# Optimization experiments

Measured on AMD Instinct MI355X. Metric: run time of the kernel, lower is better.

## Reference

```python
import jax, jax.numpy as jnp
import numpy as np

N_SIN = 3  # fcn_n_sin

def _feats(x):
    # x: [B, Din] -> features [B, Din, 1 + 2*N_SIN]
    omega = (2.0 ** jnp.arange(N_SIN, dtype=x.dtype))  # [n_sin]
    ox = x[..., None] * omega  # [B, Din, n_sin]
    return jnp.concatenate([x[..., None], jnp.sin(ox), jnp.cos(ox)], axis=-1)

def setup_inputs() -> dict:
    key = jax.random.key(0)
    k1, k2, k3 = jax.random.split(key, 3)
    B, Din, Dout, H, F = 2048, 64, 64, 32, 1 + 2 * N_SIN
    x = jax.random.normal(k1, (B, Din), dtype=jnp.float32)
    # xavier-normal-ish init for W1/W2, zeros for biases (matches init_parameters)
    W1 = jax.random.normal(k2, (Din, Dout, H, F), dtype=jnp.float32) * np.sqrt(2.0 / (H + F))
    W2 = jax.random.normal(k3, (Din, Dout, 1, H), dtype=jnp.float32) * np.sqrt(2.0 / (1 + H))
    B1 = jnp.zeros((Din, Dout, H), dtype=jnp.float32)
    B2 = jnp.zeros((Din, Dout, 1), dtype=jnp.float32)
    return {"x": x, "W1": W1, "W2": W2, "B1": B1, "B2": B2}

def reference(x, W1, W2, B1, B2):
    f = _feats(x)  # [B, Din, F]
    # per-edge first layer: [B, Din, Dout, H]
    h = jnp.einsum('bif,iohf->bioh', f, W1) + B1[None]
    h = jax.nn.silu(h)
    # per-edge second layer -> scalar: [B, Din, Dout]
    phis = jnp.einsum('bioh,ioh->bio', h, W2[:, :, 0, :]) + B2[:, :, 0][None]
    return phis.sum(axis=1)  # [B, Dout]
```

## Files before the change

### kernel.cpp

```cpp
#include <hip/hip_runtime.h>
#include <math.h>

typedef _Float16 f16;
typedef f16   f16x4    __attribute__((ext_vector_type(4)));
typedef f16   f16x8    __attribute__((ext_vector_type(8)));
typedef float floatx2  __attribute__((ext_vector_type(2)));
typedef float floatx4  __attribute__((ext_vector_type(4)));
typedef float floatx16 __attribute__((ext_vector_type(16)));

#define LOG2E   1.44269504088896340736f
#define INV_2PI 0.15915494309189533577f

#define B_SZ  2048
#define DIN   64
#define DOUT  64
#define NH    32

#define NIG   4
#define IGW   (DIN / NIG)

#define W1IMG_ELEMS ((size_t)DIN * DOUT * 64 * 4)
#define FIMG_ELEMS  ((size_t)DIN * 64 * 64 * 4)

__device__ __forceinline__ floatx2 pk_add(floatx2 a, floatx2 b) {
    floatx2 d; asm("v_pk_add_f32 %0, %1, %2" : "=v"(d) : "v"(a), "v"(b)); return d;
}
__device__ __forceinline__ floatx2 pk_mul(floatx2 a, floatx2 b) {
    floatx2 d; asm("v_pk_mul_f32 %0, %1, %2" : "=v"(d) : "v"(a), "v"(b)); return d;
}
__device__ __forceinline__ floatx2 pk_fma(floatx2 a, floatx2 b, floatx2 c) {
    floatx2 d; asm("v_pk_fma_f32 %0, %1, %2, %3" : "=v"(d) : "v"(a), "v"(b), "v"(c)); return d;
}

__global__ __launch_bounds__(256) void prep_kernel(
        const float* __restrict__ W1, const float* __restrict__ B1,
        const float* __restrict__ B2, const float* __restrict__ x,
        f16* __restrict__ w1img, f16* __restrict__ fimg,
        float* __restrict__ b2sum, float* __restrict__ out) {
    const int bid = blockIdx.x, tid = threadIdx.x;
    if (bid < 512) {
        int u = bid * 256 + tid;
        int lane2 = u & 31, o = (u >> 5) & 63, i = u >> 11;
        int l0 = lane2 * 2;
        f16x8 v;
        if (lane2 < 16) {
#pragma unroll
            for (int t = 0; t < 2; ++t) {
                const float* w = W1 + (size_t)((i * 64 + o) * 32 + l0 + t) * 7;
#pragma unroll
                for (int j = 0; j < 4; ++j) v[t * 4 + j] = (f16)(w[j] * (-LOG2E));
            }
        } else {
#pragma unroll
            for (int t = 0; t < 2; ++t) {
                int m = l0 - 32 + t;
                const float* w = W1 + (size_t)((i * 64 + o) * 32 + m) * 7;
                v[t * 4 + 0] = (f16)(w[4] * (-LOG2E));
                v[t * 4 + 1] = (f16)(w[5] * (-LOG2E));
                v[t * 4 + 2] = (f16)(w[6] * (-LOG2E));
                v[t * 4 + 3] = (f16)(B1[(i * 64 + o) * 32 + m] * (-LOG2E));
            }
        }
        *(f16x8*)(w1img + (size_t)u * 8) = v;
    } else if (bid < 1024) {
        int u = (bid - 512) * 256 + tid;
        int lane2 = u & 31, btp = (u >> 5) & 63, i = u >> 11;
        int l0 = lane2 * 2;
        f16x8 v;
#pragma unroll
        for (int t = 0; t < 2; ++t) {
            int b = btp * 32 + ((l0 + t) & 31);
            float xv = x[b * 64 + i];
            float s1 = __builtin_amdgcn_sinf(xv * INV_2PI);
            float c1 = __builtin_amdgcn_cosf(xv * INV_2PI);
            float s2 = 2.0f * s1 * c1, c2 = 1.0f - 2.0f * s1 * s1;
            float s4 = 2.0f * s2 * c2, c4 = 1.0f - 2.0f * s2 * s2;
            if (lane2 < 16) { v[t*4+0] = (f16)xv; v[t*4+1] = (f16)s1;
                              v[t*4+2] = (f16)s2; v[t*4+3] = (f16)s4; }
            else            { v[t*4+0] = (f16)c1; v[t*4+1] = (f16)c2;
                              v[t*4+2] = (f16)c4; v[t*4+3] = (f16)1.0f; }
        }
        *(f16x8*)(fimg + (size_t)u * 8) = v;
    } else if (bid < 1152) {
        int t = (bid - 1024) * 256 + tid;
        floatx4 z = {};
        *(floatx4*)(out + (size_t)t * 4) = z;
    } else if (tid < 64) {
        float s = 0.0f;
        for (int i = 0; i < 64; ++i) s += B2[i * 64 + tid];
        b2sum[tid] = s;
    }
}

__device__ __forceinline__ void silu8(
        floatx2 A0, floatx2 A1, floatx2 A2, floatx2 A3,
        floatx2 W0, floatx2 W1, floatx2 W2, floatx2 W3,
        floatx2 one2, float& phi) {
    floatx2 E0 = {__builtin_amdgcn_exp2f(A0[0]), __builtin_amdgcn_exp2f(A0[1])};
    floatx2 E1 = {__builtin_amdgcn_exp2f(A1[0]), __builtin_amdgcn_exp2f(A1[1])};
    floatx2 E2 = {__builtin_amdgcn_exp2f(A2[0]), __builtin_amdgcn_exp2f(A2[1])};
    floatx2 E3 = {__builtin_amdgcn_exp2f(A3[0]), __builtin_amdgcn_exp2f(A3[1])};
    floatx2 D0 = pk_add(E0, one2), D1 = pk_add(E1, one2);
    floatx2 D2 = pk_add(E2, one2), D3 = pk_add(E3, one2);
    floatx2 U0 = pk_mul(A0, W0), U1 = pk_mul(A1, W1);
    floatx2 U2 = pk_mul(A2, W2), U3 = pk_mul(A3, W3);
    floatx2 N01 = pk_fma(U0, D1, pk_mul(U1, D0));
    floatx2 N23 = pk_fma(U2, D3, pk_mul(U3, D2));
    floatx2 P01 = pk_mul(D0, D1), P23 = pk_mul(D2, D3);
    floatx2 N   = pk_fma(N01, P23, pk_mul(N23, P01));
    floatx2 DD  = pk_mul(P01, P23);
    float n8 = __builtin_fmaf(N[0], DD[1], N[1] * DD[0]);
    float d8 = DD[0] * DD[1];
    phi = __builtin_fmaf(n8, __builtin_amdgcn_rcpf(d8), phi);
}

__global__ __launch_bounds__(128, 6) void main_kernel(
        const f16* __restrict__ w1img, const f16* __restrict__ fimg,
        const float* __restrict__ W2, const float* __restrict__ b2sum,
        float* __restrict__ out) {
    const int tid  = threadIdx.x;
    const int lane = tid & 63;
    const int wv   = tid >> 6;
    const int btp  = blockIdx.x & 63;
    const int og   = (blockIdx.x >> 6) & 31;
    const int ig   = blockIdx.x >> 11;
    const int o    = __builtin_amdgcn_readfirstlane(og * 2 + wv);
    const int p    = lane >> 5;
    const size_t ibase = (size_t)ig * IGW;

    __shared__ float ws2[2][IGW + 1][32];
    {
        int idx = tid * 8;
        int wv_ = idx >> 9, ii_ = (idx >> 5) & 15, h_ = idx & 31;
        const float* src = W2 + (ibase + ii_) * 2048
                         + (size_t)(og * 2 + wv_) * 32 + h_;
        *(floatx4*)&ws2[wv_][ii_][h_]     = *(const floatx4*)src;
        *(floatx4*)&ws2[wv_][ii_][h_ + 4] = *(const floatx4*)(src + 4);
    }
    __syncthreads();

    const f16* ap = w1img + ibase * 16384 + ((size_t)o   * 64 + lane) * 4;
    const f16* bp = fimg  + ibase * 16384 + ((size_t)btp * 64 + lane) * 4;

    const floatx16 zeroC = {};
    const floatx2  one2  = {1.0f, 1.0f};
    float phiL = 0.0f, phiH = 0.0f;

    f16x4 a0v = *(const f16x4*)ap;
    f16x4 b0v = *(const f16x4*)bp;
    f16x4 a_n = *(const f16x4*)(ap + 16384);
    f16x4 b_n = *(const f16x4*)(bp + 16384);
    floatx16 Ccur = __builtin_amdgcn_mfma_f32_32x32x8f16(a0v, b0v, zeroC, 0, 0, 0);

#pragma unroll 2
    for (int ii = 0; ii < IGW; ++ii) {
        floatx16 Cn = __builtin_amdgcn_mfma_f32_32x32x8f16(a_n, b_n, zeroC, 0, 0, 0);
        const size_t i2 = (size_t)(ii + 2);
        a_n = *(const f16x4*)(ap + i2 * 16384);
        b_n = *(const f16x4*)(bp + i2 * 16384);

        const float* wrow = &ws2[wv][ii][p * 4];
        const floatx4 W0 = *(const floatx4*)(wrow);
        const floatx4 W1v = *(const floatx4*)(wrow + 8);
        const floatx4 W2v = *(const floatx4*)(wrow + 16);
        const floatx4 W3v = *(const floatx4*)(wrow + 24);

        silu8((floatx2){Ccur[0],  Ccur[1]},  (floatx2){Ccur[4],  Ccur[5]},
              (floatx2){Ccur[8],  Ccur[9]},  (floatx2){Ccur[12], Ccur[13]},
              (floatx2){W0[0], W0[1]}, (floatx2){W1v[0], W1v[1]},
              (floatx2){W2v[0], W2v[1]}, (floatx2){W3v[0], W3v[1]},
              one2, phiL);
        silu8((floatx2){Ccur[2],  Ccur[3]},  (floatx2){Ccur[6],  Ccur[7]},
              (floatx2){Ccur[10], Ccur[11]}, (floatx2){Ccur[14], Ccur[15]},
              (floatx2){W0[2], W0[3]}, (floatx2){W1v[2], W1v[3]},
              (floatx2){W2v[2], W2v[3]}, (floatx2){W3v[2], W3v[3]},
              one2, phiH);

        Ccur = Cn;
    }

    float phi = phiL + phiH;
    phi += __shfl_xor(phi, 32, 64);

    if (lane < 32) {
        float v = phi * (-1.0f / LOG2E) + (1.0f / NIG) * b2sum[o];
        unsafeAtomicAdd(out + (size_t)(btp * 32 + lane) * 64 + o, v);
    }
}

extern "C" void kernel_launch(void* const* d_in, const int* in_sizes, int n_in,
                              void* d_out, int out_size, void* d_ws, size_t ws_size,
                              hipStream_t stream) {
    const float* x  = (const float*)d_in[0];
    const float* W1 = (const float*)d_in[1];
    const float* W2 = (const float*)d_in[2];
    const float* B1 = (const float*)d_in[3];
    const float* B2 = (const float*)d_in[4];
    float* out = (float*)d_out;

    f16*   w1img = (f16*)d_ws;
    f16*   fimg  = w1img + W1IMG_ELEMS;
    float* b2sum = (float*)(fimg + FIMG_ELEMS);

    prep_kernel<<<1153, 256, 0, stream>>>(W1, B1, B2, x, w1img, fimg, b2sum, out);
    main_kernel<<<NIG * 32 * 64, 128, 0, stream>>>(w1img, fimg, W2, b2sum, out);
}
```

Measured before the change: 111.8 us.

## Fold W2 into a second W1 image and compute A*W2 via extra MFMA

```diff
diff --git a/kernel.cpp b/kernel.cpp
--- a/kernel.cpp
+++ b/kernel.cpp
@@ -34,36 +34,44 @@
 
 __global__ __launch_bounds__(256) void prep_kernel(
         const float* __restrict__ W1, const float* __restrict__ B1,
-        const float* __restrict__ B2, const float* __restrict__ x,
-        f16* __restrict__ w1img, f16* __restrict__ fimg,
-        float* __restrict__ b2sum, float* __restrict__ out) {
+        const float* __restrict__ W2, const float* __restrict__ B2,
+        const float* __restrict__ x,
+        f16* __restrict__ w1img, f16* __restrict__ w12img,
+        f16* __restrict__ fimg, float* __restrict__ b2sum,
+        float* __restrict__ out) {
     const int bid = blockIdx.x, tid = threadIdx.x;
-    if (bid < 512) {
-        int u = bid * 256 + tid;
+    if (bid < 1024) {
+        const bool second = bid >= 512;
+        int u = (second ? bid - 512 : bid) * 256 + tid;
         int lane2 = u & 31, o = (u >> 5) & 63, i = u >> 11;
         int l0 = lane2 * 2;
         f16x8 v;
         if (lane2 < 16) {
 #pragma unroll
             for (int t = 0; t < 2; ++t) {
-                const float* w = W1 + (size_t)((i * 64 + o) * 32 + l0 + t) * 7;
+                int m = l0 + t;
+                float sc = -LOG2E;
+                if (second) sc *= W2[(size_t)(i * 64 + o) * 32 + m];
+                const float* w = W1 + (size_t)((i * 64 + o) * 32 + m) * 7;
 #pragma unroll
-                for (int j = 0; j < 4; ++j) v[t * 4 + j] = (f16)(w[j] * (-LOG2E));
+                for (int j = 0; j < 4; ++j) v[t * 4 + j] = (f16)(w[j] * sc);
             }
         } else {
 #pragma unroll
             for (int t = 0; t < 2; ++t) {
                 int m = l0 - 32 + t;
+                float sc = -LOG2E;
+                if (second) sc *= W2[(size_t)(i * 64 + o) * 32 + m];
                 const float* w = W1 + (size_t)((i * 64 + o) * 32 + m) * 7;
-                v[t * 4 + 0] = (f16)(w[4] * (-LOG2E));
-                v[t * 4 + 1] = (f16)(w[5] * (-LOG2E));
-                v[t * 4 + 2] = (f16)(w[6] * (-LOG2E));
-                v[t * 4 + 3] = (f16)(B1[(i * 64 + o) * 32 + m] * (-LOG2E));
+                v[t * 4 + 0] = (f16)(w[4] * sc);
+                v[t * 4 + 1] = (f16)(w[5] * sc);
+                v[t * 4 + 2] = (f16)(w[6] * sc);
+                v[t * 4 + 3] = (f16)(B1[(i * 64 + o) * 32 + m] * sc);
             }
         }
-        *(f16x8*)(w1img + (size_t)u * 8) = v;
-    } else if (bid < 1024) {
-        int u = (bid - 512) * 256 + tid;
+        *(f16x8*)((second ? w12img : w1img) + (size_t)u * 8) = v;
+    } else if (bid < 1536) {
+        int u = (bid - 1024) * 256 + tid;
         int lane2 = u & 31, btp = (u >> 5) & 63, i = u >> 11;
         int l0 = lane2 * 2;
         f16x8 v;
@@ -81,8 +89,8 @@
                               v[t*4+2] = (f16)c4; v[t*4+3] = (f16)1.0f; }
         }
         *(f16x8*)(fimg + (size_t)u * 8) = v;
-    } else if (bid < 1152) {
-        int t = (bid - 1024) * 256 + tid;
+    } else if (bid < 1664) {
+        int t = (bid - 1536) * 256 + tid;
         floatx4 z = {};
         *(floatx4*)(out + (size_t)t * 4) = z;
     } else if (tid < 64) {
@@ -94,7 +102,7 @@
 
 __device__ __forceinline__ void silu8(
         floatx2 A0, floatx2 A1, floatx2 A2, floatx2 A3,
-        floatx2 W0, floatx2 W1, floatx2 W2, floatx2 W3,
+        floatx2 U0, floatx2 U1, floatx2 U2, floatx2 U3,
         floatx2 one2, float& phi) {
     floatx2 E0 = {__builtin_amdgcn_exp2f(A0[0]), __builtin_amdgcn_exp2f(A0[1])};
     floatx2 E1 = {__builtin_amdgcn_exp2f(A1[0]), __builtin_amdgcn_exp2f(A1[1])};
@@ -102,8 +110,6 @@
     floatx2 E3 = {__builtin_amdgcn_exp2f(A3[0]), __builtin_amdgcn_exp2f(A3[1])};
     floatx2 D0 = pk_add(E0, one2), D1 = pk_add(E1, one2);
     floatx2 D2 = pk_add(E2, one2), D3 = pk_add(E3, one2);
-    floatx2 U0 = pk_mul(A0, W0), U1 = pk_mul(A1, W1);
-    floatx2 U2 = pk_mul(A2, W2), U3 = pk_mul(A3, W3);
     floatx2 N01 = pk_fma(U0, D1, pk_mul(U1, D0));
     floatx2 N23 = pk_fma(U2, D3, pk_mul(U3, D2));
     floatx2 P01 = pk_mul(D0, D1), P23 = pk_mul(D2, D3);
@@ -115,8 +121,8 @@
 }
 
 __global__ __launch_bounds__(128, 6) void main_kernel(
-        const f16* __restrict__ w1img, const f16* __restrict__ fimg,
-        const float* __restrict__ W2, const float* __restrict__ b2sum,
+        const f16* __restrict__ w1img, const f16* __restrict__ w12img,
+        const f16* __restrict__ fimg, const float* __restrict__ b2sum,
         float* __restrict__ out) {
     const int tid  = threadIdx.x;
     const int lane = tid & 63;
@@ -125,58 +131,40 @@
     const int og   = (blockIdx.x >> 6) & 31;
     const int ig   = blockIdx.x >> 11;
     const int o    = __builtin_amdgcn_readfirstlane(og * 2 + wv);
-    const int p    = lane >> 5;
     const size_t ibase = (size_t)ig * IGW;
 
-    __shared__ float ws2[2][IGW + 1][32];
-    {
-        int idx = tid * 8;
-        int wv_ = idx >> 9, ii_ = (idx >> 5) & 15, h_ = idx & 31;
-        const float* src = W2 + (ibase + ii_) * 2048
-                         + (size_t)(og * 2 + wv_) * 32 + h_;
-        *(floatx4*)&ws2[wv_][ii_][h_]     = *(const floatx4*)src;
-        *(floatx4*)&ws2[wv_][ii_][h_ + 4] = *(const floatx4*)(src + 4);
-    }
-    __syncthreads();
-
-    const f16* ap = w1img + ibase * 16384 + ((size_t)o   * 64 + lane) * 4;
-    const f16* bp = fimg  + ibase * 16384 + ((size_t)btp * 64 + lane) * 4;
+    const f16* ap1 = w1img  + ibase * 16384 + ((size_t)o   * 64 + lane) * 4;
+    const f16* ap2 = w12img + ibase * 16384 + ((size_t)o   * 64 + lane) * 4;
+    const f16* bp  = fimg   + ibase * 16384 + ((size_t)btp * 64 + lane) * 4;
 
     const floatx16 zeroC = {};
     const floatx2  one2  = {1.0f, 1.0f};
     float phiL = 0.0f, phiH = 0.0f;
 
-    f16x4 a0v = *(const f16x4*)ap;
-    f16x4 b0v = *(const f16x4*)bp;
-    f16x4 a_n = *(const f16x4*)(ap + 16384);
-    f16x4 b_n = *(const f16x4*)(bp + 16384);
-    floatx16 Ccur = __builtin_amdgcn_mfma_f32_32x32x8f16(a0v, b0v, zeroC, 0, 0, 0);
+    f16x4 fa1 = *(const f16x4*)ap1;
+    f16x4 fa2 = *(const f16x4*)ap2;
+    f16x4 fb  = *(const f16x4*)bp;
 
-#pragma unroll 2
+#pragma unroll 1
     for (int ii = 0; ii < IGW; ++ii) {
-        floatx16 Cn = __builtin_amdgcn_mfma_f32_32x32x8f16(a_n, b_n, zeroC, 0, 0, 0);
-        const size_t i2 = (size_t)(ii + 2);
-        a_n = *(const f16x4*)(ap + i2 * 16384);
-        b_n = *(const f16x4*)(bp + i2 * 16384);
+        floatx16 C1 = __builtin_amdgcn_mfma_f32_32x32x8f16(fa1, fb, zeroC, 0, 0, 0);
+        floatx16 C2 = __builtin_amdgcn_mfma_f32_32x32x8f16(fa2, fb, zeroC, 0, 0, 0);
 
-        const float* wrow = &ws2[wv][ii][p * 4];
-        const floatx4 W0 = *(const floatx4*)(wrow);
-        const floatx4 W1v = *(const floatx4*)(wrow + 8);
-        const floatx4 W2v = *(const floatx4*)(wrow + 16);
-        const floatx4 W3v = *(const floatx4*)(wrow + 24);
+        const size_t i1 = (size_t)(ii + 1);
+        fa1 = *(const f16x4*)(ap1 + i1 * 16384);
+        fa2 = *(const f16x4*)(ap2 + i1 * 16384);
+        fb  = *(const f16x4*)(bp  + i1 * 16384);
 
-        silu8((floatx2){Ccur[0],  Ccur[1]},  (floatx2){Ccur[4],  Ccur[5]},
-              (floatx2){Ccur[8],  Ccur[9]},  (floatx2){Ccur[12], Ccur[13]},
-              (floatx2){W0[0], W0[1]}, (floatx2){W1v[0], W1v[1]},
-              (floatx2){W2v[0], W2v[1]}, (floatx2){W3v[0], W3v[1]},
+        silu8((floatx2){C1[0],  C1[1]},  (floatx2){C1[4],  C1[5]},
+              (floatx2){C1[8],  C1[9]},  (floatx2){C1[12], C1[13]},
+              (floatx2){C2[0],  C2[1]},  (floatx2){C2[4],  C2[5]},
+              (floatx2){C2[8],  C2[9]},  (floatx2){C2[12], C2[13]},
               one2, phiL);
-        silu8((floatx2){Ccur[2],  Ccur[3]},  (floatx2){Ccur[6],  Ccur[7]},
-              (floatx2){Ccur[10], Ccur[11]}, (floatx2){Ccur[14], Ccur[15]},
-              (floatx2){W0[2], W0[3]}, (floatx2){W1v[2], W1v[3]},
-              (floatx2){W2v[2], W2v[3]}, (floatx2){W3v[2], W3v[3]},
+        silu8((floatx2){C1[2],  C1[3]},  (floatx2){C1[6],  C1[7]},
+              (floatx2){C1[10], C1[11]}, (floatx2){C1[14], C1[15]},
+              (floatx2){C2[2],  C2[3]},  (floatx2){C2[6],  C2[7]},
+              (floatx2){C2[10], C2[11]}, (floatx2){C2[14], C2[15]},
               one2, phiH);
-
-        Ccur = Cn;
     }
 
     float phi = phiL + phiH;
@@ -198,10 +186,12 @@
     const float* B2 = (const float*)d_in[4];
     float* out = (float*)d_out;
 
-    f16*   w1img = (f16*)d_ws;
-    f16*   fimg  = w1img + W1IMG_ELEMS;
-    float* b2sum = (float*)(fimg + FIMG_ELEMS);
+    f16*   w1img  = (f16*)d_ws;
+    f16*   w12img = w1img  + W1IMG_ELEMS;
+    f16*   fimg   = w12img + W1IMG_ELEMS;
+    float* b2sum  = (float*)(fimg + FIMG_ELEMS);
 
-    prep_kernel<<<1153, 256, 0, stream>>>(W1, B1, B2, x, w1img, fimg, b2sum, out);
-    main_kernel<<<NIG * 32 * 64, 128, 0, stream>>>(w1img, fimg, W2, b2sum, out);
+    prep_kernel<<<1665, 256, 0, stream>>>(W1, B1, W2, B2, x,
+                                          w1img, w12img, fimg, b2sum, out);
+    main_kernel<<<NIG * 32 * 64, 128, 0, stream>>>(w1img, w12img, fimg, b2sum, out);
 }
```

New measurement: 111.4 us. Within noise of the previous version (-0.3%).
